# Optimization experiments

Measured on AMD Instinct MI355X. Metric: run time of the kernel, lower is better.

## Reference

```python
import jax, jax.numpy as jnp
import numpy as np

D_MODEL = 1024
HEADS = 16
D_HEAD = D_MODEL // HEADS


def setup_inputs() -> dict:
    key = jax.random.key(0)
    ks = jax.random.split(key, 12)
    B, L = 2, 2048
    s = 1.0 / np.sqrt(D_MODEL)
    inp = {
        "q": jax.random.normal(ks[0], (B, L, D_MODEL), jnp.float32),
        "k": jax.random.normal(ks[1], (B, L, D_MODEL), jnp.float32),
        "v": jax.random.normal(ks[2], (B, L, D_MODEL), jnp.float32),
        # torch nn.Linear params: weight [out, in], bias [out]
        "w_q": jax.random.normal(ks[3], (D_MODEL, D_MODEL), jnp.float32) * s,
        "b_q": jax.random.normal(ks[4], (D_MODEL,), jnp.float32) * s,
        "w_k": jax.random.normal(ks[5], (D_MODEL, D_MODEL), jnp.float32) * s,
        "b_k": jax.random.normal(ks[6], (D_MODEL,), jnp.float32) * s,
        "w_v": jax.random.normal(ks[7], (D_MODEL, D_MODEL), jnp.float32) * s,
        "b_v": jax.random.normal(ks[8], (D_MODEL,), jnp.float32) * s,
        "w_o": jax.random.normal(ks[9], (D_MODEL, D_MODEL), jnp.float32) * s,
        "b_o": jax.random.normal(ks[10], (D_MODEL,), jnp.float32) * s,
    }
    return inp


def reference(q, k, v, w_q, b_q, w_k, b_k, w_v, b_v, w_o, b_o):
    B, L, _ = q.shape
    # QKV projections (torch Linear: x @ W^T + b)
    qh = (q @ w_q.T + b_q).reshape(B, L, HEADS, D_HEAD)
    kh = (k @ w_k.T + b_k).reshape(B, L, HEADS, D_HEAD)
    vh = (v @ w_v.T + b_v).reshape(B, L, HEADS, D_HEAD)
    # scaled dot-product attention per head
    scale = 1.0 / jnp.sqrt(jnp.asarray(D_HEAD, qh.dtype))
    scores = jnp.einsum("bqhd,bkhd->bhqk", qh, kh) * scale  # [B,H,Lq,Lk]
    attn = jax.nn.softmax(scores, axis=-1)
    out = jnp.einsum("bhqk,bkhd->bqhd", attn, vh)  # [B,Lq,H,Dh]
    out = out.reshape(B, L, HEADS * D_HEAD)
    return out @ w_o.T + b_o
```

## Files before the change

### kernel.cpp

```cpp
#include <hip/hip_runtime.h>
#include <hip/hip_bf16.h>

typedef __attribute__((ext_vector_type(8))) short bf16x8;
typedef __attribute__((ext_vector_type(2))) float f32x2;
typedef __attribute__((ext_vector_type(4))) float f32x4;
typedef __attribute__((ext_vector_type(16))) float f32x16;
typedef __attribute__((ext_vector_type(2))) unsigned u32x2;
typedef __attribute__((ext_vector_type(4))) unsigned u32x4;
typedef __attribute__((ext_vector_type(4))) float float4a;

#define DEV static __device__ __forceinline__

constexpr int DM = 1024;
constexpr int NH = 16;
constexpr int DH = 64;
constexpr int BATCH = 2;
constexpr int SEQ = 2048;
constexpr int NROWS = BATCH * NH * SEQ;
constexpr float CS = 0.18033688011112042f;

DEV unsigned short f2bf(float x) {
  unsigned u = __float_as_uint(x);
  u += 0x7fff + ((u >> 16) & 1);
  return (unsigned short)(u >> 16);
}
DEV float bf2f(short h) {
  unsigned u = ((unsigned)(unsigned short)h) << 16;
  return __uint_as_float(u);
}
DEV unsigned pk2(float a, float b) {
  return (unsigned)f2bf(a) | ((unsigned)f2bf(b) << 16);
}
DEV unsigned pkrn(float a, float b) {
  union { __hip_bfloat162 h; unsigned u; } cv;
  cv.h = __float22bfloat162_rn(make_float2(a, b));
  return cv.u;
}
DEV float exp2raw(float x) { return __builtin_amdgcn_exp2f(x); }

DEV void gload16(const void* g, void* l) {
  __builtin_amdgcn_global_load_lds(
      (const __attribute__((address_space(1))) unsigned*)g,
      (__attribute__((address_space(3))) unsigned*)l, 16, 0, 0);
}

DEV u32x2 plswap(unsigned a, unsigned b) {
  auto r = __builtin_amdgcn_permlane32_swap(a, b, false, false);
  return (u32x2){(unsigned)r[0], (unsigned)r[1]};
}
DEV float xsum32(float x) {
  u32x2 r = plswap(__float_as_uint(x), __float_as_uint(x));
  return __uint_as_float(r[0]) + __uint_as_float(r[1]);
}

DEV float tree16(const f32x16& v) {
  f32x2 a0 = {v[0], v[1]},  a1 = {v[2], v[3]},  a2 = {v[4], v[5]},  a3 = {v[6], v[7]};
  f32x2 a4 = {v[8], v[9]},  a5 = {v[10], v[11]}, a6 = {v[12], v[13]}, a7 = {v[14], v[15]};
  f32x2 b0 = a0 + a1, b1 = a2 + a3, b2 = a4 + a5, b3 = a6 + a7;
  f32x2 c0 = b0 + b1, c1 = b2 + b3;
  f32x2 d = c0 + c1;
  return d[0] + d[1];
}

__global__ void cvt7_kernel(const float* s0, const float* s1, const float* s2,
                            const float* s3, const float* s4, const float* s5, const float* s6,
                            short* d0, short* d1, short* d2, short* d3,
                            short* d4, short* d5, short* d6) {
  const float* s; short* d; int n8;
  switch (blockIdx.z) {
    case 0: s = s0; d = d0; n8 = 524288; break;
    case 1: s = s1; d = d1; n8 = 524288; break;
    case 2: s = s2; d = d2; n8 = 524288; break;
    case 3: s = s3; d = d3; n8 = 131072; break;
    case 4: s = s4; d = d4; n8 = 131072; break;
    case 5: s = s5; d = d5; n8 = 131072; break;
    default: s = s6; d = d6; n8 = 131072; break;
  }
  int i = blockIdx.x * blockDim.x + threadIdx.x;
  if (i >= n8) return;
  const float4a* sp = (const float4a*)s;
  float4a a = sp[2 * i], b = sp[2 * i + 1];
  bf16x8 o;
  o[0] = (short)f2bf(a[0]); o[1] = (short)f2bf(a[1]);
  o[2] = (short)f2bf(a[2]); o[3] = (short)f2bf(a[3]);
  o[4] = (short)f2bf(b[0]); o[5] = (short)f2bf(b[1]);
  o[6] = (short)f2bf(b[2]); o[7] = (short)f2bf(b[3]);
  ((bf16x8*)d)[i] = o;
}

__global__ __launch_bounds__(256, 2)
void gemm_qkv(const short* __restrict__ A0, const short* __restrict__ A1, const short* __restrict__ A2,
              const short* __restrict__ W0, const short* __restrict__ W1, const short* __restrict__ W2,
              const float* __restrict__ bi0, const float* __restrict__ bi1, const float* __restrict__ bi2,
              short* C0, short* C1, short* C2) {
  constexpr int M = 4096, N = 1024, K = 1024;
  const int lid = blockIdx.x + (blockIdx.y << 3) + (blockIdx.z << 8);
  const int swz = (lid & 7) * 96 + (lid >> 3);
  const int zz = swz >> 8;
  const int rem = swz & 255;
  const int m0 = (rem >> 3) * 128;
  const int n0 = (rem & 7) * 128;

  const short* A = A0; const short* W = W0; const float* bias = bi0; short* C = C0;
  if (zz == 1) { A = A1; W = W1; bias = bi1; C = C1; }
  if (zz == 2) { A = A2; W = W2; bias = bi2; C = C2; }

  __shared__ short sA[128 * 64];
  __shared__ short sB[128 * 64];

  const int t = threadIdx.x;
  const int lane = t & 63;
  const int w = t >> 6;
  const int wm = w >> 1, wn = w & 1;

  f32x4 acc[4][4] = {};

  const int srow = t >> 3;
  const int schk = t & 7;

  for (int k0 = 0; k0 < K; k0 += 64) {
    __syncthreads();
#pragma unroll
    for (int r = 0; r < 4; ++r) {
      int row = r * 32 + srow;
      int cl = schk ^ (row & 7);
      gload16(A + (size_t)(m0 + row) * K + k0 + cl * 8,
              (char*)sA + r * 4096 + w * 1024);
      gload16(W + (size_t)(n0 + row) * K + k0 + cl * 8,
              (char*)sB + r * 4096 + w * 1024);
    }
    __syncthreads();
#pragma unroll
    for (int ks = 0; ks < 2; ++ks) {
      bf16x8 af[4], bfr[4];
#pragma unroll
      for (int f = 0; f < 4; ++f) {
        int ra = wm * 64 + f * 16 + (lane & 15);
        int ca = (ks * 4 + (lane >> 4)) ^ (ra & 7);
        af[f] = *(const bf16x8*)((const char*)sA + ra * 128 + ca * 16);
        int rb = wn * 64 + f * 16 + (lane & 15);
        int cb2 = (ks * 4 + (lane >> 4)) ^ (rb & 7);
        bfr[f] = *(const bf16x8*)((const char*)sB + rb * 128 + cb2 * 16);
      }
#pragma unroll
      for (int mf = 0; mf < 4; ++mf)
#pragma unroll
        for (int nf = 0; nf < 4; ++nf)
          acc[mf][nf] = __builtin_amdgcn_mfma_f32_16x16x32_bf16(af[mf], bfr[nf], acc[mf][nf], 0, 0, 0);
    }
  }

  const int cb = n0 + wn * 64 + (lane & 15);
  const int rb = m0 + wm * 64 + ((lane >> 4) << 2);
  const float sc = (zz == 0) ? CS : 1.0f;
  if (zz == 2) {
#pragma unroll
    for (int nf = 0; nf < 4; ++nf) {
      float bv = bias[cb + nf * 16];
#pragma unroll
      for (int mf = 0; mf < 4; ++mf) {
        u32x2 pr;
        pr[0] = pk2(acc[mf][nf][0] + bv, acc[mf][nf][1] + bv);
        pr[1] = pk2(acc[mf][nf][2] + bv, acc[mf][nf][3] + bv);
        *(u32x2*)(C + (size_t)(cb + nf * 16) * M + rb + mf * 16) = pr;
      }
    }
  } else {
#pragma unroll
    for (int nf = 0; nf < 4; ++nf) {
      float bv = bias[cb + nf * 16];
#pragma unroll
      for (int mf = 0; mf < 4; ++mf) {
#pragma unroll
        for (int j = 0; j < 4; ++j) {
          float vv = (acc[mf][nf][j] + bv) * sc;
          C[(size_t)(rb + mf * 16 + j) * N + cb + nf * 16] = (short)f2bf(vv);
        }
      }
    }
  }
}

__global__ __launch_bounds__(256, 2)
void gemm_out(const short* __restrict__ A, const short* __restrict__ W,
              const float* __restrict__ bias, float* __restrict__ C) {
  constexpr int M = 4096, N = 1024, K = 1024;
  const int lid = blockIdx.x + (blockIdx.y << 4);
  const int swz = (lid & 7) * 64 + (lid >> 3);
  const int n0 = (swz & 15) * 64;
  const int m0 = (swz >> 4) * 128;

  __shared__ short sA[128 * 64];
  __shared__ short sB[64 * 64];

  const int t = threadIdx.x;
  const int lane = t & 63;
  const int w = t >> 6;
  const int wm = w >> 1, wn = w & 1;

  f32x4 acc[4][2] = {};

  const int srow = t >> 3;
  const int schk = t & 7;

  for (int k0 = 0; k0 < K; k0 += 64) {
    __syncthreads();
#pragma unroll
    for (int r = 0; r < 4; ++r) {
      int row = r * 32 + srow;
      int cl = schk ^ (row & 7);
      gload16(A + (size_t)(m0 + row) * K + k0 + cl * 8,
              (char*)sA + r * 4096 + w * 1024);
    }
#pragma unroll
    for (int r = 0; r < 2; ++r) {
      int row = r * 32 + srow;
      int cl = schk ^ (row & 7);
      gload16(W + (size_t)(n0 + row) * K + k0 + cl * 8,
              (char*)sB + r * 4096 + w * 1024);
    }
    __syncthreads();
#pragma unroll
    for (int ks = 0; ks < 2; ++ks) {
      bf16x8 af[4], bfr[2];
#pragma unroll
      for (int f = 0; f < 4; ++f) {
        int ra = wm * 64 + f * 16 + (lane & 15);
        int ca = (ks * 4 + (lane >> 4)) ^ (ra & 7);
        af[f] = *(const bf16x8*)((const char*)sA + ra * 128 + ca * 16);
      }
#pragma unroll
      for (int f = 0; f < 2; ++f) {
        int rb = wn * 32 + f * 16 + (lane & 15);
        int cb2 = (ks * 4 + (lane >> 4)) ^ (rb & 7);
        bfr[f] = *(const bf16x8*)((const char*)sB + rb * 128 + cb2 * 16);
      }
#pragma unroll
      for (int mf = 0; mf < 4; ++mf)
#pragma unroll
        for (int nf = 0; nf < 2; ++nf)
          acc[mf][nf] = __builtin_amdgcn_mfma_f32_16x16x32_bf16(af[mf], bfr[nf], acc[mf][nf], 0, 0, 0);
    }
  }

  const int cb = n0 + wn * 32 + (lane & 15);
  const int rb = m0 + wm * 64 + ((lane >> 4) << 2);
#pragma unroll
  for (int nf = 0; nf < 2; ++nf) {
    float bv = bias[cb + nf * 16];
#pragma unroll
    for (int mf = 0; mf < 4; ++mf)
#pragma unroll
      for (int j = 0; j < 4; ++j)
        C[(size_t)(rb + mf * 16 + j) * N + cb + nf * 16] = acc[mf][nf][j] + bv;
  }
}

__global__ __launch_bounds__(256, 4)
void attn_kernel(const short* __restrict__ qh, const short* __restrict__ kh,
                 const short* __restrict__ vt,
                 short* __restrict__ po0, short* __restrict__ po1,
                 short* __restrict__ po2, short* __restrict__ po3,
                 float* __restrict__ pl) {
  const int lid = blockIdx.x + (blockIdx.y << 4) + (blockIdx.z << 9);
  const int swz = (lid & 7) * 256 + (lid >> 3);
  const int qt = swz & 15;
  const int bh = (swz >> 4) & 31;
  const int sp = swz >> 9;

  const int b = bh >> 4, h = bh & 15;
  const int q0 = qt * 128;
  const int kvbase = sp * (SEQ / 4);
  const int t = threadIdx.x;
  const int lane = t & 63;
  const int w = t >> 6;
  const int hi = lane >> 5, l31 = lane & 31;

  __shared__ short sK[2][4096];
  __shared__ short sVt[2][4096];

  bf16x8 qf[4];
  {
    const short* qp = qh + ((size_t)b * SEQ + q0 + w * 32 + l31) * DM + h * DH + hi * 8;
#pragma unroll
    for (int ks = 0; ks < 4; ++ks) qf[ks] = *(const bf16x8*)(qp + ks * 16);
  }

  f32x16 o0 = {}, o1 = {};
  float l = 0.f;

  const short* kB = kh + ((size_t)b * SEQ) * DM + h * DH;
  const short* vtB = vt + (size_t)(h * DH) * (BATCH * SEQ) + b * SEQ;

  int c_row[2], c_off[2];
#pragma unroll
  for (int half = 0; half < 2; ++half) {
    int c = half * 256 + t;
    c_row[half] = c >> 3;
    c_off[half] = ((c & 7) ^ ((c >> 3) & 7)) * 8;
  }

  auto stage = [&](int buf, int kv0) {
#pragma unroll
    for (int half = 0; half < 2; ++half) {
      gload16(kB + (size_t)(kv0 + c_row[half]) * DM + c_off[half],
              (char*)&sK[buf][0] + half * 4096 + w * 1024);
      gload16(vtB + (size_t)c_row[half] * (BATCH * SEQ) + kv0 + c_off[half],
              (char*)&sVt[buf][0] + half * 4096 + w * 1024);
    }
  };

  stage(0, kvbase);
  __syncthreads();

  constexpr int NT = (SEQ / 4) / 64;
  for (int tt = 0; tt < NT; ++tt) {
    const int cur = tt & 1;
    if (tt + 1 < NT) stage(cur ^ 1, kvbase + (tt + 1) * 64);

    f32x16 s0 = {}, s1 = {};
    {
      const char* kbase = (const char*)&sK[cur][0];
      __builtin_amdgcn_s_setprio(1);
#pragma unroll
      for (int ks = 0; ks < 4; ++ks) {
        int ch = ((ks * 2 + hi) ^ (l31 & 7)) * 16;
        bf16x8 a0 = *(const bf16x8*)(kbase + l31 * 128 + ch);
        bf16x8 a1 = *(const bf16x8*)(kbase + (32 + l31) * 128 + ch);
        s0 = __builtin_amdgcn_mfma_f32_32x32x16_bf16(a0, qf[ks], s0, 0, 0, 0);
        s1 = __builtin_amdgcn_mfma_f32_32x32x16_bf16(a1, qf[ks], s1, 0, 0, 0);
      }
      __builtin_amdgcn_s_setprio(0);
    }

#pragma unroll
    for (int r = 0; r < 16; ++r) s0[r] = exp2raw(s0[r]);
#pragma unroll
    for (int r = 0; r < 16; ++r) s1[r] = exp2raw(s1[r]);
    l += tree16(s0) + tree16(s1);

    union U { u32x4 u; bf16x8 h; };
    bf16x8 pa[4];
#pragma unroll
    for (int ks = 0; ks < 4; ++ks) {
      const f32x16 sv = (ks < 2) ? s0 : s1;
      const int ro = (ks & 1) * 8;
      unsigned u0 = pkrn(sv[ro + 0], sv[ro + 1]);
      unsigned u1 = pkrn(sv[ro + 2], sv[ro + 3]);
      unsigned u2 = pkrn(sv[ro + 4], sv[ro + 5]);
      unsigned u3 = pkrn(sv[ro + 6], sv[ro + 7]);
      u32x2 r02 = plswap(u0, u2);
      u32x2 r13 = plswap(u1, u3);
      U pu;
      pu.u = (u32x4){r02[0], r13[0], r02[1], r13[1]};
      pa[ks] = pu.h;
    }

    {
      const char* vbase = (const char*)&sVt[cur][0];
      __builtin_amdgcn_s_setprio(1);
#pragma unroll
      for (int ks = 0; ks < 4; ++ks) {
        int ch = ((ks * 2 + hi) ^ (l31 & 7)) * 16;
        bf16x8 vb0 = *(const bf16x8*)(vbase + l31 * 128 + ch);
        bf16x8 vb1 = *(const bf16x8*)(vbase + (32 + l31) * 128 + ch);
        o0 = __builtin_amdgcn_mfma_f32_32x32x16_bf16(pa[ks], vb0, o0, 0, 0, 0);
        o1 = __builtin_amdgcn_mfma_f32_32x32x16_bf16(pa[ks], vb1, o1, 0, 0, 0);
      }
      __builtin_amdgcn_s_setprio(0);
    }

    __syncthreads();
  }

  const int rowbase = (bh << 11) + q0 + w * 32;
  float lt = xsum32(l);
  if (lane < 32) pl[sp * NROWS + rowbase + lane] = lt;
  short* pb = (sp & 2) ? ((sp & 1) ? po3 : po2) : ((sp & 1) ? po1 : po0);
#pragma unroll
  for (int r = 0; r < 16; ++r) {
    int qr = (r & 3) + 8 * (r >> 2) + 4 * hi;
    size_t base = (size_t)(rowbase + qr) * 64 + l31;
    pb[base]      = (short)f2bf(o0[r]);
    pb[base + 32] = (short)f2bf(o1[r]);
  }
}

__global__ void combine_kernel(const short* __restrict__ po0, const short* __restrict__ po1,
                               const short* __restrict__ po2, const short* __restrict__ po3,
                               const float* __restrict__ pl,
                               short* __restrict__ ao) {
  int idx = blockIdx.x * 256 + threadIdx.x;
  int row = idx >> 3, d8 = (idx & 7) * 8;
  float inv = 1.0f / (pl[row] + pl[NROWS + row] + pl[2 * NROWS + row] + pl[3 * NROWS + row]);
  bf16x8 a = *(const bf16x8*)(po0 + (size_t)row * 64 + d8);
  bf16x8 b = *(const bf16x8*)(po1 + (size_t)row * 64 + d8);
  bf16x8 c = *(const bf16x8*)(po2 + (size_t)row * 64 + d8);
  bf16x8 d = *(const bf16x8*)(po3 + (size_t)row * 64 + d8);
  int bh = row >> 11, q = row & 2047;
  int bb = bh >> 4, hh = bh & 15;
  short* dst = ao + ((size_t)bb * SEQ + q) * DM + hh * DH + d8;
  bf16x8 o;
#pragma unroll
  for (int e = 0; e < 8; ++e)
    o[e] = (short)f2bf(((bf2f(a[e]) + bf2f(b[e])) + (bf2f(c[e]) + bf2f(d[e]))) * inv);
  *(bf16x8*)dst = o;
}

extern "C" void kernel_launch(void* const* d_in, const int* in_sizes, int n_in,
                              void* d_out, int out_size, void* d_ws, size_t ws_size,
                              hipStream_t stream) {
  (void)in_sizes; (void)n_in; (void)out_size; (void)ws_size;
  const float* q   = (const float*)d_in[0];
  const float* k   = (const float*)d_in[1];
  const float* v   = (const float*)d_in[2];
  const float* w_q = (const float*)d_in[3];
  const float* b_q = (const float*)d_in[4];
  const float* w_k = (const float*)d_in[5];
  const float* b_k = (const float*)d_in[6];
  const float* w_v = (const float*)d_in[7];
  const float* b_v = (const float*)d_in[8];
  const float* w_o = (const float*)d_in[9];
  const float* b_o = (const float*)d_in[10];

  char* ws = (char*)d_ws;
  const size_t MB = 1u << 20;
  short* qb  = (short*)(ws + 0 * MB);
  short* kb  = (short*)(ws + 8 * MB);
  short* vb  = (short*)(ws + 16 * MB);
  short* wqb = (short*)(ws + 24 * MB);
  short* wkb = (short*)(ws + 26 * MB);
  short* wvb = (short*)(ws + 28 * MB);
  short* wob = (short*)(ws + 30 * MB);
  short* qhb = (short*)(ws + 32 * MB);
  short* khb = (short*)(ws + 40 * MB);
  short* vtb = (short*)(ws + 48 * MB);
  short* po0 = (short*)(ws + 0 * MB);
  short* po1 = (short*)(ws + 8 * MB);
  short* po2 = (short*)(ws + 16 * MB);
  short* po3 = (short*)(ws + 56 * MB);
  float* pl  = (float*)(ws + 24 * MB);
  short* aob = (short*)(ws + 32 * MB);

  dim3 gc(2048, 1, 7);
  cvt7_kernel<<<gc, 256, 0, stream>>>(q, k, v, w_q, w_k, w_v, w_o,
                                      qb, kb, vb, wqb, wkb, wvb, wob);

  dim3 gq(1024 / 128, 4096 / 128, 3);
  gemm_qkv<<<gq, 256, 0, stream>>>(qb, kb, vb, wqb, wkb, wvb,
                                   b_q, b_k, b_v, qhb, khb, vtb);

  dim3 ga(SEQ / 128, BATCH * NH, 4);
  attn_kernel<<<ga, 256, 0, stream>>>(qhb, khb, vtb, po0, po1, po2, po3, pl);

  combine_kernel<<<(NROWS * 8) / 256, 256, 0, stream>>>(po0, po1, po2, po3, pl, aob);

  dim3 go(1024 / 64, 4096 / 128, 1);
  gemm_out<<<go, 256, 0, stream>>>(aob, wob, b_o, (float*)d_out);
}
```

Measured before the change: 121.9 us.

## Fuse split-KV combine into output projection GEMM A-tile loading

Removes the separate combine kernel and makes the output GEMM merge the four partial attention outputs and normalise by the summed row sums while staging A tiles into shared memory. The partial-sum layout is changed to interleave the four split values per row so they load as one vector. This removes a kernel launch and the write and re-read of the combined activation buffer. In exchange, each output-GEMM block re-reads four partial buffers per A tile and does the combine math redundantly across the column tiles, and it replaces asynchronous global-to-LDS loads with register loads.

```diff
diff --git a/kernel.cpp b/kernel.cpp
--- a/kernel.cpp
+++ b/kernel.cpp
@@ -182,7 +182,10 @@
 }
 
 __global__ __launch_bounds__(256, 2)
-void gemm_out(const short* __restrict__ A, const short* __restrict__ W,
+void gemm_out(const short* __restrict__ po0, const short* __restrict__ po1,
+              const short* __restrict__ po2, const short* __restrict__ po3,
+              const float* __restrict__ pl,
+              const short* __restrict__ W,
               const float* __restrict__ bias, float* __restrict__ C) {
   constexpr int M = 4096, N = 1024, K = 1024;
   const int lid = blockIdx.x + (blockIdx.y << 4);
@@ -206,18 +209,36 @@
   for (int k0 = 0; k0 < K; k0 += 64) {
     __syncthreads();
 #pragma unroll
-    for (int r = 0; r < 4; ++r) {
-      int row = r * 32 + srow;
-      int cl = schk ^ (row & 7);
-      gload16(A + (size_t)(m0 + row) * K + k0 + cl * 8,
-              (char*)sA + r * 4096 + w * 1024);
-    }
-#pragma unroll
     for (int r = 0; r < 2; ++r) {
       int row = r * 32 + srow;
       int cl = schk ^ (row & 7);
       gload16(W + (size_t)(n0 + row) * K + k0 + cl * 8,
               (char*)sB + r * 4096 + w * 1024);
+    }
+#pragma unroll
+    for (int r = 0; r < 4; ++r) {
+      int row = r * 32 + srow;
+      int gr  = m0 + row;
+      int cl  = schk ^ (row & 7);
+      int col = k0 + cl * 8;
+      size_t prow = ((size_t)((gr >> 11) * 16 + (col >> 6)) << 11) + (gr & 2047);
+      size_t pidx = prow * 64 + (col & 63);
+      bf16x8 pa_ = *(const bf16x8*)(po0 + pidx);
+      bf16x8 pb_ = *(const bf16x8*)(po1 + pidx);
+      bf16x8 pc_ = *(const bf16x8*)(po2 + pidx);
+      bf16x8 pd_ = *(const bf16x8*)(po3 + pidx);
+      float4a plv = *(const float4a*)(pl + prow * 4);
+      float inv = 1.0f / ((plv[0] + plv[1]) + (plv[2] + plv[3]));
+      u32x4 pk;
+#pragma unroll
+      for (int e = 0; e < 4; ++e) {
+        float lo = ((bf2f(pa_[2 * e]) + bf2f(pb_[2 * e])) +
+                    (bf2f(pc_[2 * e]) + bf2f(pd_[2 * e]))) * inv;
+        float hv = ((bf2f(pa_[2 * e + 1]) + bf2f(pb_[2 * e + 1])) +
+                    (bf2f(pc_[2 * e + 1]) + bf2f(pd_[2 * e + 1]))) * inv;
+        pk[e] = pkrn(lo, hv);
+      }
+      *(u32x4*)((char*)sA + row * 128 + schk * 16) = pk;
     }
     __syncthreads();
 #pragma unroll
@@ -375,7 +396,7 @@
 
   const int rowbase = (bh << 11) + q0 + w * 32;
   float lt = xsum32(l);
-  if (lane < 32) pl[sp * NROWS + rowbase + lane] = lt;
+  if (lane < 32) pl[(size_t)(rowbase + lane) * 4 + sp] = lt;
   short* pb = (sp & 2) ? ((sp & 1) ? po3 : po2) : ((sp & 1) ? po1 : po0);
 #pragma unroll
   for (int r = 0; r < 16; ++r) {
@@ -384,27 +405,6 @@
     pb[base]      = (short)f2bf(o0[r]);
     pb[base + 32] = (short)f2bf(o1[r]);
   }
-}
-
-__global__ void combine_kernel(const short* __restrict__ po0, const short* __restrict__ po1,
-                               const short* __restrict__ po2, const short* __restrict__ po3,
-                               const float* __restrict__ pl,
-                               short* __restrict__ ao) {
-  int idx = blockIdx.x * 256 + threadIdx.x;
-  int row = idx >> 3, d8 = (idx & 7) * 8;
-  float inv = 1.0f / (pl[row] + pl[NROWS + row] + pl[2 * NROWS + row] + pl[3 * NROWS + row]);
-  bf16x8 a = *(const bf16x8*)(po0 + (size_t)row * 64 + d8);
-  bf16x8 b = *(const bf16x8*)(po1 + (size_t)row * 64 + d8);
-  bf16x8 c = *(const bf16x8*)(po2 + (size_t)row * 64 + d8);
-  bf16x8 d = *(const bf16x8*)(po3 + (size_t)row * 64 + d8);
-  int bh = row >> 11, q = row & 2047;
-  int bb = bh >> 4, hh = bh & 15;
-  short* dst = ao + ((size_t)bb * SEQ + q) * DM + hh * DH + d8;
-  bf16x8 o;
-#pragma unroll
-  for (int e = 0; e < 8; ++e)
-    o[e] = (short)f2bf(((bf2f(a[e]) + bf2f(b[e])) + (bf2f(c[e]) + bf2f(d[e]))) * inv);
-  *(bf16x8*)dst = o;
 }
 
 extern "C" void kernel_launch(void* const* d_in, const int* in_sizes, int n_in,
@@ -440,7 +440,6 @@
   short* po2 = (short*)(ws + 16 * MB);
   short* po3 = (short*)(ws + 56 * MB);
   float* pl  = (float*)(ws + 24 * MB);
-  short* aob = (short*)(ws + 32 * MB);
 
   dim3 gc(2048, 1, 7);
   cvt7_kernel<<<gc, 256, 0, stream>>>(q, k, v, w_q, w_k, w_v, w_o,
@@ -453,8 +452,6 @@
   dim3 ga(SEQ / 128, BATCH * NH, 4);
   attn_kernel<<<ga, 256, 0, stream>>>(qhb, khb, vtb, po0, po1, po2, po3, pl);
 
-  combine_kernel<<<(NROWS * 8) / 256, 256, 0, stream>>>(po0, po1, po2, po3, pl, aob);
-
   dim3 go(1024 / 64, 4096 / 128, 1);
-  gemm_out<<<go, 256, 0, stream>>>(aob, wob, b_o, (float*)d_out);
-}
+  gemm_out<<<go, 256, 0, stream>>>(po0, po1, po2, po3, pl, wob, b_o, (float*)d_out);
+}
```

New measurement: 164.0 us. 34.5% more time.
